# Optimization experiments

Hardware: AMD Instinct MI355X
Metric: run time of the kernel (lower is better)

The kernel has to match this reference:

```python
import jax, jax.numpy as jnp
import numpy as np

NUM_HEADS = 8
D_MODEL = 256
DIM = D_MODEL // NUM_HEADS  # 32
EPS = 1e-6


def _proj(x, W, b):
    # Conv1d with kernel_size=1 == channel-mixing matmul over length axis
    return jnp.einsum('oi,bil->bol', W, x) + b[None, :, None]


def _linear_attention(q, k, v):
    # q,k,v: [B, dim, heads, L]
    q = jax.nn.elu(q) + 1.0
    k = jax.nn.elu(k) + 1.0
    L = v.shape[3]
    v = v / L
    # KV: [B, dim_v, dim_k, heads]
    KV = jnp.einsum('bdhm,bqhm->bqdh', k, v)
    # Z: [B, heads, L]
    Z = 1.0 / (jnp.einsum('bdhm,bdh->bhm', q, k.sum(3)) + EPS)
    # out: [B, dim, heads, L]
    return jnp.einsum('bdhm,bqdh,bhm->bqhm', q, KV, Z) * L


def setup_inputs() -> dict:
    key = jax.random.key(0)
    ks = jax.random.split(key, 11)
    B, L = 8, 4096
    s = 0.05
    return {
        'query': jax.random.normal(ks[0], (B, D_MODEL, L), dtype=jnp.float32),
        'key':   jax.random.normal(ks[1], (B, D_MODEL, L), dtype=jnp.float32),
        'value': jax.random.normal(ks[2], (B, D_MODEL, L), dtype=jnp.float32),
        'Wq': jax.random.normal(ks[3], (D_MODEL, D_MODEL), dtype=jnp.float32) * s,
        'bq': jnp.zeros((D_MODEL,), dtype=jnp.float32),
        'Wk': jax.random.normal(ks[4], (D_MODEL, D_MODEL), dtype=jnp.float32) * s,
        'bk': jnp.zeros((D_MODEL,), dtype=jnp.float32),
        'Wv': jax.random.normal(ks[5], (D_MODEL, D_MODEL), dtype=jnp.float32) * s,
        'bv': jnp.zeros((D_MODEL,), dtype=jnp.float32),
        'Wm': jax.random.normal(ks[6], (D_MODEL, D_MODEL), dtype=jnp.float32) * s,
        'bm': jnp.zeros((D_MODEL,), dtype=jnp.float32),
    }


def reference(query, key, value, Wq, bq, Wk, bk, Wv, bv, Wm, bm):
    B = query.shape[0]
    q = _proj(query, Wq, bq).reshape(B, DIM, NUM_HEADS, -1)
    k = _proj(key,   Wk, bk).reshape(B, DIM, NUM_HEADS, -1)
    v = _proj(value, Wv, bv).reshape(B, DIM, NUM_HEADS, -1)
    x = _linear_attention(q, k, v)           # [B, dim, heads, L]
    x = x.reshape(B, D_MODEL, -1)            # merge heads back to channels
    return jnp.einsum('oi,bil->bol', Wm, x) + bm[None, :, None]
```

## Files before the change

### kernel.cpp

```cpp
#include <hip/hip_runtime.h>
#include <math.h>

#define D_MODEL 256
#define NHEADS 8
#define HDIM 32
#define BATCH 8
#define SEQL 4096
#define EPS 1e-6f

typedef _Float16 f16;
typedef _Float16 f16x4 __attribute__((ext_vector_type(4)));
typedef _Float16 f16x8 __attribute__((ext_vector_type(8)));
typedef float f32x4 __attribute__((ext_vector_type(4)));

__device__ __forceinline__ float elu1(float x) {
    return x > 0.f ? x + 1.f : __expf(x);
}

__global__ void prep_kernel(const float* __restrict__ Wq, const float* __restrict__ Wk,
                            const float* __restrict__ Wv, const float* __restrict__ Wm,
                            const float* __restrict__ bq, const float* __restrict__ bk,
                            const float* __restrict__ bv,
                            f16* __restrict__ w16, float* __restrict__ bperm) {
    const int bid = blockIdx.x;
    if (bid < 1024) {
        int idx = bid * 256 + threadIdx.x;
        int mat = idx >> 16, r = (idx >> 8) & 255, c = idx & 255;
        const float* W = (mat == 0) ? Wq : (mat == 1) ? Wk : (mat == 2) ? Wv : Wm;
        float v;
        if (mat < 3) v = W[(size_t)(((r & 31) << 3) + (r >> 5)) * 256 + c];
        else         v = W[(size_t)r * 256 + (((c & 31) << 3) + (c >> 5))];
        w16[idx] = (f16)v;
    } else {
        int t = threadIdx.x;
        bperm[0 * 256 + t] = bq[((t & 31) << 3) + (t >> 5)];
        bperm[1 * 256 + t] = bk[((t & 31) << 3) + (t >> 5)];
        bperm[2 * 256 + t] = bv[((t & 31) << 3) + (t >> 5)];
    }
}

#define BSTR 40
__global__ __launch_bounds__(256, 3) void gemm_stage1(
    const float* __restrict__ Xq, const float* __restrict__ Xk, const float* __restrict__ Xv,
    const f16* __restrict__ w16, const float* __restrict__ bperm,
    f16* __restrict__ yq, f16* __restrict__ yk, f16* __restrict__ yv) {
    __shared__ __align__(16) char smem[20480];
    f16* B0 = (f16*)smem;
    f16* B1 = (f16*)smem + 128 * BSTR;
    f16* Cb = (f16*)smem;

    const int z = blockIdx.z;
    const int which = z >> 3;
    const int b = z & 7;
    const float* X = (which == 0) ? Xq : (which == 1) ? Xk : Xv;
    const f16* W = w16 + which * 65536;
    f16* Y = (which == 0) ? yq : (which == 1) ? yk : yv;
    const float* bp = bperm + which * 256;

    const int l0 = blockIdx.x * 128;
    const int m0 = blockIdx.y * 128;
    const int tid = threadIdx.x;
    const int wave = tid >> 6, lane = tid & 63;
    const int wm = wave >> 1, wn = wave & 1;
    const int ln = lane & 15, quad = lane >> 4;
    const int bp8 = tid & 7;
    const int bg = tid >> 3;

    const float* Xbase = X + ((size_t)b * D_MODEL + 4 * bp8) * SEQL + l0 + 4 * bg;
    const f16* Wb[4];
#pragma unroll
    for (int mf = 0; mf < 4; ++mf)
        Wb[mf] = W + (size_t)(m0 + wm * 64 + mf * 16 + ln) * 256 + quad * 8;

    float4 xa[4], xb[4];
    f16x8 afc[4], afn[4];

#define LOADX(DST, K0) do { \
        const float* xb_ = Xbase + (size_t)(K0) * SEQL; \
        DST[0] = *(const float4*)(xb_ + 0 * SEQL); \
        DST[1] = *(const float4*)(xb_ + 1 * SEQL); \
        DST[2] = *(const float4*)(xb_ + 2 * SEQL); \
        DST[3] = *(const float4*)(xb_ + 3 * SEQL); \
    } while (0)

#define STOREB(SRC, BUF) do { \
        f16x4 w_; \
        w_[0] = (f16)SRC[0].x; w_[1] = (f16)SRC[1].x; w_[2] = (f16)SRC[2].x; w_[3] = (f16)SRC[3].x; \
        *(f16x4*)&BUF[(4 * bg + 0) * BSTR + 4 * bp8] = w_; \
        w_[0] = (f16)SRC[0].y; w_[1] = (f16)SRC[1].y; w_[2] = (f16)SRC[2].y; w_[3] = (f16)SRC[3].y; \
        *(f16x4*)&BUF[(4 * bg + 1) * BSTR + 4 * bp8] = w_; \
        w_[0] = (f16)SRC[0].z; w_[1] = (f16)SRC[1].z; w_[2] = (f16)SRC[2].z; w_[3] = (f16)SRC[3].z; \
        *(f16x4*)&BUF[(4 * bg + 2) * BSTR + 4 * bp8] = w_; \
        w_[0] = (f16)SRC[0].w; w_[1] = (f16)SRC[1].w; w_[2] = (f16)SRC[2].w; w_[3] = (f16)SRC[3].w; \
        *(f16x4*)&BUF[(4 * bg + 3) * BSTR + 4 * bp8] = w_; \
    } while (0)

    f32x4 acc[4][4];
#pragma unroll
    for (int mf = 0; mf < 4; ++mf)
#pragma unroll
        for (int nf = 0; nf < 4; ++nf)
#pragma unroll
            for (int r = 0; r < 4; ++r) acc[mf][nf][r] = 0.f;

    LOADX(xa, 0);
#pragma unroll
    for (int mf = 0; mf < 4; ++mf) afc[mf] = *(const f16x8*)(Wb[mf] + 0);

#pragma unroll
    for (int it = 0; it < 8; ++it) {
        const int k0 = it * 32;
        f16* buf = (it & 1) ? B1 : B0;
        if (it < 7) {
            if (it & 1) LOADX(xa, k0 + 32);
            else        LOADX(xb, k0 + 32);
        }
        if (it & 1) STOREB(xb, buf);
        else        STOREB(xa, buf);
        __syncthreads();
        if (it < 7) {
#pragma unroll
            for (int mf = 0; mf < 4; ++mf)
                afn[mf] = *(const f16x8*)(Wb[mf] + k0 + 32);
        }
        f16x8 bf[4];
#pragma unroll
        for (int nf = 0; nf < 4; ++nf)
            bf[nf] = *(const f16x8*)&buf[(wn * 64 + nf * 16 + ln) * BSTR + quad * 8];
#pragma unroll
        for (int mf = 0; mf < 4; ++mf)
#pragma unroll
            for (int nf = 0; nf < 4; ++nf)
                acc[mf][nf] = __builtin_amdgcn_mfma_f32_16x16x32_f16(afc[mf], bf[nf], acc[mf][nf], 0, 0, 0);
#pragma unroll
        for (int mf = 0; mf < 4; ++mf) afc[mf] = afn[mf];
    }

    float bv_[4][4];
#pragma unroll
    for (int mf = 0; mf < 4; ++mf)
#pragma unroll
        for (int r = 0; r < 4; ++r)
            bv_[mf][r] = bp[m0 + wm * 64 + mf * 16 + quad * 4 + r];
#pragma unroll
    for (int pass = 0; pass < 2; ++pass) {
        __syncthreads();
        if (wm == pass) {
#pragma unroll
            for (int mf = 0; mf < 4; ++mf)
#pragma unroll
                for (int nf = 0; nf < 4; ++nf) {
                    const int olocal = mf * 16 + quad * 4;
                    const int llocal = wn * 64 + nf * 16 + ln;
                    f16x4 w;
#pragma unroll
                    for (int r = 0; r < 4; ++r) w[r] = (f16)(acc[mf][nf][r] + bv_[mf][r]);
                    *(f16x4*)&Cb[llocal * 72 + olocal] = w;
                }
        }
        __syncthreads();
        const int l = tid >> 1, half = tid & 1;
        f16* yr = Y + ((size_t)(b * SEQL + l0 + l)) * 256 + m0 + pass * 64 + half * 32;
#pragma unroll
        for (int u = 0; u < 4; ++u)
            *(f16x8*)(yr + u * 8) = *(const f16x8*)&Cb[l * 72 + half * 32 + u * 8];
    }
#undef LOADX
#undef STOREB
}

#define KVLP 66
__global__ __launch_bounds__(256) void kv_mfma(
    const f16* __restrict__ kp, const f16* __restrict__ vp,
    float* __restrict__ KVpart, float* __restrict__ ksum_part) {
    __shared__ __align__(16) f16 kT[32 * KVLP];
    __shared__ __align__(16) f16 vT[48 * KVLP];
    const int ls = blockIdx.x;
    const int bh = blockIdx.y;
    const int b = bh >> 3, h = bh & 7;
    const int t = threadIdx.x;
    const int wave = t >> 6, lane = t & 63;
    const int ln = lane & 15, quad = lane >> 4;
    const int lrow = t >> 2, seg = t & 3;

    {
        const int rr = 32 + (t >> 4), c0 = (t & 15) * 4;
        f16x4 w;
        const f16 one = (f16)1.f, zero = (f16)0.f;
        w[0] = w[1] = w[2] = w[3] = (rr == 32) ? one : zero;
        *(f16x4*)&vT[rr * KVLP + c0] = w;
    }

    const int tiP = wave >> 1, tjP = wave & 1;
    f32x4 accP, accS;
#pragma unroll
    for (int r = 0; r < 4; ++r) { accP[r] = 0.f; accS[r] = 0.f; }

    for (int ch = 0; ch < 8; ++ch) {
        __syncthreads();
        const size_t goff = ((size_t)(b * SEQL + ls * 512 + ch * 64 + lrow)) * 256 + h * 32 + seg * 8;
        f16x8 k8 = *(const f16x8*)(kp + goff);
        f16x8 v8 = *(const f16x8*)(vp + goff);
#pragma unroll
        for (int j = 0; j < 8; ++j) {
            kT[(seg * 8 + j) * KVLP + lrow] = (f16)elu1((float)k8[j]);
            vT[(seg * 8 + j) * KVLP + lrow] = v8[j];
        }
        __syncthreads();
#pragma unroll
        for (int ks = 0; ks < 2; ++ks) {
            const int kc = ks * 32 + quad * 8;
            f16x8 bP = *(const f16x8*)&kT[(tjP * 16 + ln) * KVLP + kc];
            f16x8 aP = *(const f16x8*)&vT[(tiP * 16 + ln) * KVLP + kc];
            accP = __builtin_amdgcn_mfma_f32_16x16x32_f16(aP, bP, accP, 0, 0, 0);
            if (wave < 2) {
                f16x8 aS = *(const f16x8*)&vT[(32 + ln) * KVLP + kc];
                accS = __builtin_amdgcn_mfma_f32_16x16x32_f16(aS, bP, accS, 0, 0, 0);
            }
        }
    }

    float* KVp = KVpart + ((size_t)ls * 64 + bh) * 1024;
#pragma unroll
    for (int r = 0; r < 4; ++r)
        KVp[(tiP * 16 + quad * 4 + r) * 32 + tjP * 16 + ln] = accP[r];
    if (wave < 2 && quad == 0)
        ksum_part[((size_t)ls * 64 + bh) * 32 + tjP * 16 + ln] = accS[0];
}

__global__ __launch_bounds__(256) void attn_out_kernel(
    const f16* __restrict__ qp, const float* __restrict__ KVpart,
    const float* __restrict__ ksum_part, const f16* __restrict__ wm16,
    const float* __restrict__ bm, float* __restrict__ out) {
    __shared__ __align__(16) f16 xs[64 * 264];
    __shared__ __align__(16) f16 Baug[8 * 48 * 40];
    __shared__ float dens[8][64];
    const int b = blockIdx.y;
    const int l0 = blockIdx.x * 64;
    const int t = threadIdx.x;
    const int wave = t >> 6, lane = t & 63;
    const int ln = lane & 15, quad = lane >> 4;

    {
        const int h = t >> 5, qd = t & 31;
        const float* kvp = KVpart + (size_t)(b * NHEADS + h) * 1024 + qd * 32;
        f16* dst = &Baug[(h * 48 + qd) * 40];
#pragma unroll
        for (int i = 0; i < 32; i += 4) {
            float ax = 0.f, ay = 0.f, az = 0.f, aw = 0.f;
#pragma unroll
            for (int s = 0; s < 8; ++s) {
                float4 p = *(const float4*)(kvp + (size_t)s * 65536 + i);
                ax += p.x; ay += p.y; az += p.z; aw += p.w;
            }
            f16x4 w4;
            w4[0] = (f16)ax; w4[1] = (f16)ay; w4[2] = (f16)az; w4[3] = (f16)aw;
            *(f16x4*)(dst + i) = w4;
        }
        float ksv = 0.f;
#pragma unroll
        for (int s = 0; s < 8; ++s)
            ksv += ksum_part[((size_t)s * 64 + b * NHEADS + h) * 32 + qd];
        Baug[(h * 48 + 32) * 40 + qd] = (f16)ksv;
    }
    {
        const int row = t & 63, cg = t >> 6;
        const f16* qr = qp + ((size_t)(b * SEQL + l0 + row)) * 256 + cg * 64;
        f16* dst = &xs[row * 264 + cg * 64];
#pragma unroll
        for (int u = 0; u < 64; u += 8) {
            f16x8 v = *(const f16x8*)(qr + u);
            f16x8 w;
#pragma unroll
            for (int j = 0; j < 8; ++j) w[j] = (f16)elu1((float)v[j]);
            *(f16x8*)(dst + u) = w;
        }
    }
    __syncthreads();
#pragma unroll
    for (int hh = 0; hh < 2; ++hh) {
        const int h = wave * 2 + hh;
        f16x8 a_s[4], b_s[3];
#pragma unroll
        for (int mf = 0; mf < 4; ++mf)
            a_s[mf] = *(const f16x8*)&xs[(mf * 16 + ln) * 264 + h * 32 + quad * 8];
#pragma unroll
        for (int nf = 0; nf < 3; ++nf)
            b_s[nf] = *(const f16x8*)&Baug[(h * 48 + nf * 16 + ln) * 40 + quad * 8];
        f32x4 C[4][3];
#pragma unroll
        for (int mf = 0; mf < 4; ++mf)
#pragma unroll
            for (int nf = 0; nf < 3; ++nf) {
#pragma unroll
                for (int r = 0; r < 4; ++r) C[mf][nf][r] = 0.f;
                C[mf][nf] = __builtin_amdgcn_mfma_f32_16x16x32_f16(a_s[mf], b_s[nf], C[mf][nf], 0, 0, 0);
            }
        if (ln == 0) {
#pragma unroll
            for (int mf = 0; mf < 4; ++mf)
#pragma unroll
                for (int r = 0; r < 4; ++r)
                    dens[h][mf * 16 + quad * 4 + r] = C[mf][2][r];
        }
        __syncthreads();
#pragma unroll
        for (int mf = 0; mf < 4; ++mf)
#pragma unroll
            for (int r = 0; r < 4; ++r) {
                const int l = mf * 16 + quad * 4 + r;
                const float rd = __builtin_amdgcn_rcpf(dens[h][l] + EPS);
#pragma unroll
                for (int nf = 0; nf < 2; ++nf)
                    xs[l * 264 + h * 32 + nf * 16 + ln] = (f16)(C[mf][nf][r] * rd);
            }
        __syncthreads();
    }
    f32x4 acc[4][4];
#pragma unroll
    for (int mf = 0; mf < 4; ++mf)
#pragma unroll
        for (int nf = 0; nf < 4; ++nf)
#pragma unroll
            for (int r = 0; r < 4; ++r) acc[mf][nf][r] = 0.f;
    const f16* Wb[4];
#pragma unroll
    for (int mf = 0; mf < 4; ++mf)
        Wb[mf] = wm16 + (size_t)(wave * 64 + mf * 16 + ln) * 256 + quad * 8;
    f16x8 afc[4], afn[4];
#pragma unroll
    for (int mf = 0; mf < 4; ++mf) afc[mf] = *(const f16x8*)(Wb[mf] + 0);
#pragma unroll
    for (int it = 0; it < 8; ++it) {
        const int k0 = it * 32;
        if (it < 7) {
#pragma unroll
            for (int mf = 0; mf < 4; ++mf) afn[mf] = *(const f16x8*)(Wb[mf] + k0 + 32);
        }
        f16x8 bf[4];
#pragma unroll
        for (int nf = 0; nf < 4; ++nf)
            bf[nf] = *(const f16x8*)&xs[(nf * 16 + ln) * 264 + k0 + quad * 8];
#pragma unroll
        for (int mf = 0; mf < 4; ++mf)
#pragma unroll
            for (int nf = 0; nf < 4; ++nf)
                acc[mf][nf] = __builtin_amdgcn_mfma_f32_16x16x32_f16(afc[mf], bf[nf], acc[mf][nf], 0, 0, 0);
#pragma unroll
        for (int mf = 0; mf < 4; ++mf) afc[mf] = afn[mf];
    }
#pragma unroll
    for (int mf = 0; mf < 4; ++mf) {
        const int o = wave * 64 + mf * 16 + quad * 4;
#pragma unroll
        for (int r = 0; r < 4; ++r) {
            const float bb = bm[o + r];
            float* op = out + ((size_t)(b * D_MODEL + o + r)) * SEQL + l0;
#pragma unroll
            for (int nf = 0; nf < 4; ++nf)
                op[nf * 16 + ln] = acc[mf][nf][r] + bb;
        }
    }
}

extern "C" void kernel_launch(void* const* d_in, const int* in_sizes, int n_in,
                              void* d_out, int out_size, void* d_ws, size_t ws_size,
                              hipStream_t stream) {
    const float* query = (const float*)d_in[0];
    const float* key_  = (const float*)d_in[1];
    const float* value = (const float*)d_in[2];
    const float* Wq = (const float*)d_in[3];
    const float* bq = (const float*)d_in[4];
    const float* Wk = (const float*)d_in[5];
    const float* bk = (const float*)d_in[6];
    const float* Wv = (const float*)d_in[7];
    const float* bv = (const float*)d_in[8];
    const float* Wm = (const float*)d_in[9];
    const float* bm = (const float*)d_in[10];

    char* w = (char*)d_ws;
    f16*   w16    = (f16*)w;
    float* bperm  = (float*)(w + 524288);
    float* KVpart = (float*)(w + 528384);
    float* ksum_p = (float*)(w + 2625536);
    f16*   qp     = (f16*)(w + 2691072);
    f16*   kp     = qp + (size_t)BATCH * SEQL * 256;
    f16*   vp     = kp + (size_t)BATCH * SEQL * 256;

    prep_kernel<<<1025, 256, 0, stream>>>(Wq, Wk, Wv, Wm, bq, bk, bv, w16, bperm);

    gemm_stage1<<<dim3(SEQL / 128, 2, 24), 256, 0, stream>>>(
        query, key_, value, w16, bperm, qp, kp, vp);

    kv_mfma<<<dim3(8, BATCH * NHEADS), 256, 0, stream>>>(kp, vp, KVpart, ksum_p);

    attn_out_kernel<<<dim3(SEQL / 64, BATCH), 256, 0, stream>>>(
        qp, KVpart, ksum_p, w16 + 3 * 65536, bm, (float*)d_out);
}
```

Measured before the change: 232.4 us.

## Retile projection GEMM to full-M per block and pre-reduce KV partials

The projection GEMM now stages a whole 64-column by 256-channel X tile in shared memory once and has each wave compute 64 output channels, so every input element is read from global memory once instead of twice (previously two M-blocks each re-read X). A separate kv_reduce kernel sums the eight KV and k-sum partials once per (batch, head) instead of every attention-output block redoing the reduction. This removes redundant global traffic and loads, at the cost of an extra kernel launch, a larger shared-memory tile that may lower occupancy, and less double-buffering overlap in the GEMM.

```diff
diff --git a/kernel.cpp b/kernel.cpp
--- a/kernel.cpp
+++ b/kernel.cpp
@@ -39,15 +39,13 @@
     }
 }
 
-#define BSTR 40
+#define XSTR 264
 __global__ __launch_bounds__(256, 3) void gemm_stage1(
     const float* __restrict__ Xq, const float* __restrict__ Xk, const float* __restrict__ Xv,
     const f16* __restrict__ w16, const float* __restrict__ bperm,
     f16* __restrict__ yq, f16* __restrict__ yk, f16* __restrict__ yv) {
-    __shared__ __align__(16) char smem[20480];
-    f16* B0 = (f16*)smem;
-    f16* B1 = (f16*)smem + 128 * BSTR;
-    f16* Cb = (f16*)smem;
+    __shared__ __align__(16) f16 Xs[64 * XSTR];
+    f16* Cb = Xs;
 
     const int z = blockIdx.z;
     const int which = z >> 3;
@@ -57,42 +55,35 @@
     f16* Y = (which == 0) ? yq : (which == 1) ? yk : yv;
     const float* bp = bperm + which * 256;
 
-    const int l0 = blockIdx.x * 128;
-    const int m0 = blockIdx.y * 128;
+    const int l0 = blockIdx.x * 64;
     const int tid = threadIdx.x;
     const int wave = tid >> 6, lane = tid & 63;
-    const int wm = wave >> 1, wn = wave & 1;
     const int ln = lane & 15, quad = lane >> 4;
-    const int bp8 = tid & 7;
-    const int bg = tid >> 3;
-
-    const float* Xbase = X + ((size_t)b * D_MODEL + 4 * bp8) * SEQL + l0 + 4 * bg;
-    const f16* Wb[4];
-#pragma unroll
-    for (int mf = 0; mf < 4; ++mf)
-        Wb[mf] = W + (size_t)(m0 + wm * 64 + mf * 16 + ln) * 256 + quad * 8;
+    const int kq = tid & 15;
+    const int lg = tid >> 4;
+
+    const float* Xbase = X + ((size_t)(b * D_MODEL) + 4 * kq) * SEQL + l0 + 4 * lg;
 
     float4 xa[4], xb[4];
-    f16x8 afc[4], afn[4];
-
-#define LOADX(DST, K0) do { \
-        const float* xb_ = Xbase + (size_t)(K0) * SEQL; \
-        DST[0] = *(const float4*)(xb_ + 0 * SEQL); \
-        DST[1] = *(const float4*)(xb_ + 1 * SEQL); \
-        DST[2] = *(const float4*)(xb_ + 2 * SEQL); \
-        DST[3] = *(const float4*)(xb_ + 3 * SEQL); \
+
+#define LOADX(DST, C) do { \
+        const float* xp_ = Xbase + (size_t)(64 * (C)) * SEQL; \
+        DST[0] = *(const float4*)(xp_ + 0 * SEQL); \
+        DST[1] = *(const float4*)(xp_ + 1 * SEQL); \
+        DST[2] = *(const float4*)(xp_ + 2 * SEQL); \
+        DST[3] = *(const float4*)(xp_ + 3 * SEQL); \
     } while (0)
 
-#define STOREB(SRC, BUF) do { \
+#define STOREB(SRC, C) do { \
         f16x4 w_; \
         w_[0] = (f16)SRC[0].x; w_[1] = (f16)SRC[1].x; w_[2] = (f16)SRC[2].x; w_[3] = (f16)SRC[3].x; \
-        *(f16x4*)&BUF[(4 * bg + 0) * BSTR + 4 * bp8] = w_; \
+        *(f16x4*)&Xs[(4 * lg + 0) * XSTR + 64 * (C) + 4 * kq] = w_; \
         w_[0] = (f16)SRC[0].y; w_[1] = (f16)SRC[1].y; w_[2] = (f16)SRC[2].y; w_[3] = (f16)SRC[3].y; \
-        *(f16x4*)&BUF[(4 * bg + 1) * BSTR + 4 * bp8] = w_; \
+        *(f16x4*)&Xs[(4 * lg + 1) * XSTR + 64 * (C) + 4 * kq] = w_; \
         w_[0] = (f16)SRC[0].z; w_[1] = (f16)SRC[1].z; w_[2] = (f16)SRC[2].z; w_[3] = (f16)SRC[3].z; \
-        *(f16x4*)&BUF[(4 * bg + 2) * BSTR + 4 * bp8] = w_; \
+        *(f16x4*)&Xs[(4 * lg + 2) * XSTR + 64 * (C) + 4 * kq] = w_; \
         w_[0] = (f16)SRC[0].w; w_[1] = (f16)SRC[1].w; w_[2] = (f16)SRC[2].w; w_[3] = (f16)SRC[3].w; \
-        *(f16x4*)&BUF[(4 * bg + 3) * BSTR + 4 * bp8] = w_; \
+        *(f16x4*)&Xs[(4 * lg + 3) * XSTR + 64 * (C) + 4 * kq] = w_; \
     } while (0)
 
     f32x4 acc[4][4];
@@ -104,21 +95,26 @@
             for (int r = 0; r < 4; ++r) acc[mf][nf][r] = 0.f;
 
     LOADX(xa, 0);
+    LOADX(xb, 1);
+    STOREB(xa, 0);
+    LOADX(xa, 2);
+    STOREB(xb, 1);
+    LOADX(xb, 3);
+    STOREB(xa, 2);
+    STOREB(xb, 3);
+    __syncthreads();
+
+    const f16* Wb[4];
+#pragma unroll
+    for (int mf = 0; mf < 4; ++mf)
+        Wb[mf] = W + (size_t)(wave * 64 + mf * 16 + ln) * 256 + quad * 8;
+    f16x8 afc[4], afn[4];
 #pragma unroll
     for (int mf = 0; mf < 4; ++mf) afc[mf] = *(const f16x8*)(Wb[mf] + 0);
-
-#pragma unroll
-    for (int it = 0; it < 8; ++it) {
-        const int k0 = it * 32;
-        f16* buf = (it & 1) ? B1 : B0;
-        if (it < 7) {
-            if (it & 1) LOADX(xa, k0 + 32);
-            else        LOADX(xb, k0 + 32);
-        }
-        if (it & 1) STOREB(xb, buf);
-        else        STOREB(xa, buf);
-        __syncthreads();
-        if (it < 7) {
+#pragma unroll
+    for (int s = 0; s < 8; ++s) {
+        const int k0 = s * 32;
+        if (s < 7) {
 #pragma unroll
             for (int mf = 0; mf < 4; ++mf)
                 afn[mf] = *(const f16x8*)(Wb[mf] + k0 + 32);
@@ -126,7 +122,7 @@
         f16x8 bf[4];
 #pragma unroll
         for (int nf = 0; nf < 4; ++nf)
-            bf[nf] = *(const f16x8*)&buf[(wn * 64 + nf * 16 + ln) * BSTR + quad * 8];
+            bf[nf] = *(const f16x8*)&Xs[(nf * 16 + ln) * XSTR + k0 + quad * 8];
 #pragma unroll
         for (int mf = 0; mf < 4; ++mf)
 #pragma unroll
@@ -141,29 +137,24 @@
     for (int mf = 0; mf < 4; ++mf)
 #pragma unroll
         for (int r = 0; r < 4; ++r)
-            bv_[mf][r] = bp[m0 + wm * 64 + mf * 16 + quad * 4 + r];
-#pragma unroll
-    for (int pass = 0; pass < 2; ++pass) {
-        __syncthreads();
-        if (wm == pass) {
-#pragma unroll
-            for (int mf = 0; mf < 4; ++mf)
-#pragma unroll
-                for (int nf = 0; nf < 4; ++nf) {
-                    const int olocal = mf * 16 + quad * 4;
-                    const int llocal = wn * 64 + nf * 16 + ln;
-                    f16x4 w;
-#pragma unroll
-                    for (int r = 0; r < 4; ++r) w[r] = (f16)(acc[mf][nf][r] + bv_[mf][r]);
-                    *(f16x4*)&Cb[llocal * 72 + olocal] = w;
-                }
-        }
-        __syncthreads();
-        const int l = tid >> 1, half = tid & 1;
-        f16* yr = Y + ((size_t)(b * SEQL + l0 + l)) * 256 + m0 + pass * 64 + half * 32;
-#pragma unroll
-        for (int u = 0; u < 4; ++u)
-            *(f16x8*)(yr + u * 8) = *(const f16x8*)&Cb[l * 72 + half * 32 + u * 8];
+            bv_[mf][r] = bp[wave * 64 + mf * 16 + quad * 4 + r];
+    __syncthreads();
+#pragma unroll
+    for (int mf = 0; mf < 4; ++mf)
+#pragma unroll
+        for (int nf = 0; nf < 4; ++nf) {
+            f16x4 w;
+#pragma unroll
+            for (int r = 0; r < 4; ++r) w[r] = (f16)(acc[mf][nf][r] + bv_[mf][r]);
+            *(f16x4*)&Cb[(nf * 16 + ln) * XSTR + wave * 64 + mf * 16 + quad * 4] = w;
+        }
+    __syncthreads();
+    {
+        const int l = tid >> 2, sg = tid & 3;
+        f16* yr = Y + ((size_t)(b * SEQL + l0 + l)) * 256 + sg * 64;
+#pragma unroll
+        for (int u = 0; u < 8; ++u)
+            *(f16x8*)(yr + u * 8) = *(const f16x8*)&Cb[l * XSTR + sg * 64 + u * 8];
     }
 #undef LOADX
 #undef STOREB
@@ -228,9 +219,32 @@
         ksum_part[((size_t)ls * 64 + bh) * 32 + tjP * 16 + ln] = accS[0];
 }
 
+__global__ __launch_bounds__(256) void kv_reduce(
+    const float* __restrict__ KVpart, const float* __restrict__ ksum_part,
+    float* __restrict__ KVfin, float* __restrict__ ksum_f) {
+    const int bh = blockIdx.x;
+    const int t = threadIdx.x;
+    const float* src = KVpart + (size_t)bh * 1024 + t * 4;
+    float ax = 0.f, ay = 0.f, az = 0.f, aw = 0.f;
+#pragma unroll
+    for (int s = 0; s < 8; ++s) {
+        float4 p = *(const float4*)(src + (size_t)s * 65536);
+        ax += p.x; ay += p.y; az += p.z; aw += p.w;
+    }
+    float4 o; o.x = ax; o.y = ay; o.z = az; o.w = aw;
+    *(float4*)(KVfin + (size_t)bh * 1024 + t * 4) = o;
+    if (t < 32) {
+        float ss = 0.f;
+#pragma unroll
+        for (int s = 0; s < 8; ++s)
+            ss += ksum_part[((size_t)s * 64 + bh) * 32 + t];
+        ksum_f[bh * 32 + t] = ss;
+    }
+}
+
 __global__ __launch_bounds__(256) void attn_out_kernel(
-    const f16* __restrict__ qp, const float* __restrict__ KVpart,
-    const float* __restrict__ ksum_part, const f16* __restrict__ wm16,
+    const f16* __restrict__ qp, const float* __restrict__ KV,
+    const float* __restrict__ ksum, const f16* __restrict__ wm16,
     const float* __restrict__ bm, float* __restrict__ out) {
     __shared__ __align__(16) f16 xs[64 * 264];
     __shared__ __align__(16) f16 Baug[8 * 48 * 40];
@@ -243,25 +257,16 @@
 
     {
         const int h = t >> 5, qd = t & 31;
-        const float* kvp = KVpart + (size_t)(b * NHEADS + h) * 1024 + qd * 32;
+        const float* kvp = KV + ((size_t)(b * NHEADS + h) * HDIM + qd) * HDIM;
         f16* dst = &Baug[(h * 48 + qd) * 40];
 #pragma unroll
         for (int i = 0; i < 32; i += 4) {
-            float ax = 0.f, ay = 0.f, az = 0.f, aw = 0.f;
-#pragma unroll
-            for (int s = 0; s < 8; ++s) {
-                float4 p = *(const float4*)(kvp + (size_t)s * 65536 + i);
-                ax += p.x; ay += p.y; az += p.z; aw += p.w;
-            }
+            float4 a = *(const float4*)(kvp + i);
             f16x4 w4;
-            w4[0] = (f16)ax; w4[1] = (f16)ay; w4[2] = (f16)az; w4[3] = (f16)aw;
+            w4[0] = (f16)a.x; w4[1] = (f16)a.y; w4[2] = (f16)a.z; w4[3] = (f16)a.w;
             *(f16x4*)(dst + i) = w4;
         }
-        float ksv = 0.f;
-#pragma unroll
-        for (int s = 0; s < 8; ++s)
-            ksv += ksum_part[((size_t)s * 64 + b * NHEADS + h) * 32 + qd];
-        Baug[(h * 48 + 32) * 40 + qd] = (f16)ksv;
+        Baug[(h * 48 + 32) * 40 + qd] = (f16)ksum[(size_t)(b * NHEADS + h) * HDIM + qd];
     }
     {
         const int row = t & 63, cg = t >> 6;
@@ -383,17 +388,21 @@
     float* bperm  = (float*)(w + 524288);
     float* KVpart = (float*)(w + 528384);
     float* ksum_p = (float*)(w + 2625536);
-    f16*   qp     = (f16*)(w + 2691072);
+    float* KVfin  = (float*)(w + 2691072);
+    float* ksum_f = (float*)(w + 2953216);
+    f16*   qp     = (f16*)(w + 2961408);
     f16*   kp     = qp + (size_t)BATCH * SEQL * 256;
     f16*   vp     = kp + (size_t)BATCH * SEQL * 256;
 
     prep_kernel<<<1025, 256, 0, stream>>>(Wq, Wk, Wv, Wm, bq, bk, bv, w16, bperm);
 
-    gemm_stage1<<<dim3(SEQL / 128, 2, 24), 256, 0, stream>>>(
+    gemm_stage1<<<dim3(SEQL / 64, 1, 24), 256, 0, stream>>>(
         query, key_, value, w16, bperm, qp, kp, vp);
 
     kv_mfma<<<dim3(8, BATCH * NHEADS), 256, 0, stream>>>(kp, vp, KVpart, ksum_p);
 
+    kv_reduce<<<dim3(BATCH * NHEADS), 256, 0, stream>>>(KVpart, ksum_p, KVfin, ksum_f);
+
     attn_out_kernel<<<dim3(SEQL / 64, BATCH), 256, 0, stream>>>(
-        qp, KVpart, ksum_p, w16 + 3 * 65536, bm, (float*)d_out);
-}
+        qp, KVfin, ksum_f, w16 + 3 * 65536, bm, (float*)d_out);
+}
```

After: 213.2 us. 8.3% less time.
